# Optimization experiments

Measured on AMD Instinct MI355X. Metric: run time of the kernel, lower is better.

## Reference

```python
import jax, jax.numpy as jnp
import numpy as np

VOCAB, D, TYPES = 100000, 128, 128
T, B = 409600, 8192

def setup_inputs() -> dict:
    key = jax.random.key(0)
    k1, k2, k3, k4 = jax.random.split(key, 4)
    feature_seq = jax.random.randint(k1, (T,), 0, VOCAB, dtype=jnp.int64 if jax.config.read('jax_enable_x64') else jnp.int32)
    offset_seq = jnp.sort(jax.random.randint(k2, (B,), 0, T, dtype=feature_seq.dtype))
    offset_seq = offset_seq.at[0].set(0)  # torch EmbeddingBag requires offsets[0] == 0
    W = jax.random.normal(k3, (VOCAB, D), dtype=jnp.float32) * 0.1
    L = jax.random.normal(k4, (TYPES, 2 * D), dtype=jnp.float32) * 0.05
    return {"feature_seq": feature_seq, "offset_seq": offset_seq, "W": W, "L": L}

def reference(feature_seq, offset_seq, W, L):
    n_tok = feature_seq.shape[0]
    n_bag = offset_seq.shape[0]
    # map each token position to its bag id (offsets are sorted bag starts)
    seg = jnp.searchsorted(offset_seq, jnp.arange(n_tok), side='right') - 1  # [T]
    emb = W[feature_seq]                                                     # [T, D] gather
    counts = jax.ops.segment_sum(jnp.ones((n_tok,), W.dtype), seg, num_segments=n_bag)  # [B]
    ssum = jax.ops.segment_sum(emb, seg, num_segments=n_bag)                 # [B, D]
    mean = ssum / jnp.maximum(counts, 1.0)[:, None]
    smax = jax.ops.segment_max(emb, seg, num_segments=n_bag)                 # [B, D]
    smax = jnp.where(counts[:, None] > 0, smax, 0.0)                         # empty bags -> 0
    men = jnp.concatenate([mean, smax], axis=-1)                             # [B, 2D]
    # dropout is identity in eval mode; linear has no bias
    return men @ L.T                                                         # [B, TYPES]
```

## Files before the change

kernel.cpp:

```cpp
#include <hip/hip_runtime.h>
#include <cfloat>


constexpr int D     = 128;
constexpr int TYPES = 128;
constexpr int BPB   = 4;
constexpr int WPB   = 2;
constexpr int BLOCK = 512;

__global__ __launch_bounds__(BLOCK, 8)
void embbag_men_linear(const int* __restrict__ feat,
                       const int* __restrict__ offs,
                       const float* __restrict__ W,
                       const float* __restrict__ L,
                       float* __restrict__ out,
                       int T, int B)
{
    __shared__ float4 men[BPB][64];
    __shared__ float4 redS[BPB][WPB][32];
    __shared__ float4 redM[BPB][WPB][32];
    __shared__ float  partial[3][BPB][TYPES];

    const int tid  = threadIdx.x;
    const int wv   = tid >> 6;
    const int lane = tid & 63;
    const int bi   = wv >> 1;
    const int wh   = wv & 1;
    const int slot = lane >> 5;
    const int g    = lane & 31;
    const int bag0 = blockIdx.x * BPB;
    const int bag  = bag0 + bi;

    int start = 0, end = 0;
    if (bag < B) {
        start = offs[bag];
        end   = (bag + 1 < B) ? offs[bag + 1] : T;
    }
    const int n  = end - start;
    const int q  = wh * 2 + slot;
    const int qa = start + (n * q) / 4;
    const int qb = start + (n * (q + 1)) / 4;

    float4 s4 = make_float4(0.f, 0.f, 0.f, 0.f);
    float4 m4 = make_float4(-FLT_MAX, -FLT_MAX, -FLT_MAX, -FLT_MAX);
    const float* __restrict__ Wg = W + 4 * g;

    int i = qa;
    for (; i + 8 <= qb; i += 8) {
        int idx[8];
        #pragma unroll
        for (int j = 0; j < 8; ++j) idx[j] = feat[i + j];
        float4 v[8];
        #pragma unroll
        for (int j = 0; j < 8; ++j)
            v[j] = *reinterpret_cast<const float4*>(Wg + (size_t)idx[j] * D);
        #pragma unroll
        for (int j = 0; j < 8; ++j) {
            s4.x += v[j].x; s4.y += v[j].y; s4.z += v[j].z; s4.w += v[j].w;
            m4.x = fmaxf(m4.x, v[j].x); m4.y = fmaxf(m4.y, v[j].y);
            m4.z = fmaxf(m4.z, v[j].z); m4.w = fmaxf(m4.w, v[j].w);
        }
    }
    for (; i < qb; ++i) {
        const int idx = feat[i];
        const float4 v = *reinterpret_cast<const float4*>(Wg + (size_t)idx * D);
        s4.x += v.x; s4.y += v.y; s4.z += v.z; s4.w += v.w;
        m4.x = fmaxf(m4.x, v.x); m4.y = fmaxf(m4.y, v.y);
        m4.z = fmaxf(m4.z, v.z); m4.w = fmaxf(m4.w, v.w);
    }

    s4.x += __shfl_xor(s4.x, 32); s4.y += __shfl_xor(s4.y, 32);
    s4.z += __shfl_xor(s4.z, 32); s4.w += __shfl_xor(s4.w, 32);
    m4.x = fmaxf(m4.x, __shfl_xor(m4.x, 32));
    m4.y = fmaxf(m4.y, __shfl_xor(m4.y, 32));
    m4.z = fmaxf(m4.z, __shfl_xor(m4.z, 32));
    m4.w = fmaxf(m4.w, __shfl_xor(m4.w, 32));

    if (lane < 32) {
        redS[bi][wh][g] = s4;
        redM[bi][wh][g] = m4;
    }
    __syncthreads();

    if (wh == 0 && lane < 32) {
        const float4 a0 = redS[bi][0][g], a1 = redS[bi][1][g];
        const float4 b0 = redM[bi][0][g], b1 = redM[bi][1][g];
        const bool  empty = (n <= 0);
        const float inv   = 1.0f / (float)(empty ? 1 : n);
        men[bi][g] = make_float4((a0.x + a1.x) * inv, (a0.y + a1.y) * inv,
                                 (a0.z + a1.z) * inv, (a0.w + a1.w) * inv);
        men[bi][32 + g] = empty
            ? make_float4(0.f, 0.f, 0.f, 0.f)
            : make_float4(fmaxf(b0.x, b1.x), fmaxf(b0.y, b1.y),
                          fmaxf(b0.z, b1.z), fmaxf(b0.w, b1.w));
    }
    __syncthreads();

    const int o = tid & (TYPES - 1);
    const int h = tid >> 7;

    float acc[BPB];
    #pragma unroll
    for (int b = 0; b < BPB; ++b) acc[b] = 0.f;

    const float* Lrow = L + (size_t)o * (2 * D) + h * 64;
    #pragma unroll
    for (int k4 = 0; k4 < 16; ++k4) {
        const float4 lv = *reinterpret_cast<const float4*>(Lrow + 4 * k4);
        #pragma unroll
        for (int b = 0; b < BPB; ++b) {
            const float4 mv = men[b][h * 16 + k4];
            acc[b] = fmaf(lv.x, mv.x, acc[b]);
            acc[b] = fmaf(lv.y, mv.y, acc[b]);
            acc[b] = fmaf(lv.z, mv.z, acc[b]);
            acc[b] = fmaf(lv.w, mv.w, acc[b]);
        }
    }

    if (h > 0) {
        #pragma unroll
        for (int b = 0; b < BPB; ++b) partial[h - 1][b][o] = acc[b];
    }
    __syncthreads();
    if (h == 0) {
        #pragma unroll
        for (int b = 0; b < BPB; ++b) {
            const int bg = bag0 + b;
            if (bg < B)
                out[(size_t)bg * TYPES + o] =
                    acc[b] + partial[0][b][o] + partial[1][b][o] + partial[2][b][o];
        }
    }
}

extern "C" void kernel_launch(void* const* d_in, const int* in_sizes, int n_in,
                              void* d_out, int out_size, void* d_ws, size_t ws_size,
                              hipStream_t stream)
{
    const int*   feat = (const int*)d_in[0];
    const int*   offs = (const int*)d_in[1];
    const float* W    = (const float*)d_in[2];
    const float* L    = (const float*)d_in[3];
    float*       out  = (float*)d_out;

    const int T = in_sizes[0];
    const int B = in_sizes[1];
    const int grid = (B + BPB - 1) / BPB;
    embbag_men_linear<<<grid, BLOCK, 0, stream>>>(feat, offs, W, L, out, T, B);
}
```

Measured before the change: 67.06 us.

## Split into token-parallel gather with atomics and separate linear kernel

Replaces the bag-per-block fused kernel with a three-step pipeline. A memset clears the workspace, then a token-parallel gather kernel gives each wave 64 tokens, walks bag boundaries, and accumulates sum and max into workspace through atomicAdd and an ordered-integer atomicMax. A second kernel computes the mean and max vectors and applies the linear layer, handling 8 bags per block. The aim is to fix load imbalance from uneven bag sizes, at the cost of atomic traffic, extra workspace round trips and two extra launches. The old fused kernel stays as a fallback when the workspace is too small.

```diff
diff --git a/kernel.cpp b/kernel.cpp
--- a/kernel.cpp
+++ b/kernel.cpp
@@ -4,61 +4,213 @@
 
 constexpr int D     = 128;
 constexpr int TYPES = 128;
-constexpr int BPB   = 4;
-constexpr int WPB   = 2;
-constexpr int BLOCK = 512;
-
-__global__ __launch_bounds__(BLOCK, 8)
-void embbag_men_linear(const int* __restrict__ feat,
-                       const int* __restrict__ offs,
-                       const float* __restrict__ W,
-                       const float* __restrict__ L,
-                       float* __restrict__ out,
-                       int T, int B)
+constexpr int TPW   = 64;
+constexpr int K2BPB = 8;
+
+__device__ __forceinline__ unsigned fkey(float f) {
+    unsigned b = __float_as_uint(f);
+    return (b & 0x80000000u) ? ~b : (b | 0x80000000u);
+}
+__device__ __forceinline__ float funkey(unsigned k) {
+    return __uint_as_float((k & 0x80000000u) ? (k & 0x7FFFFFFFu) : ~k);
+}
+
+__global__ __launch_bounds__(256, 8)
+void k1_gather(const int* __restrict__ feat, const int* __restrict__ offs,
+               const float* __restrict__ W,
+               float* __restrict__ wsum, unsigned* __restrict__ wkey,
+               int T, int B)
 {
-    __shared__ float4 men[BPB][64];
-    __shared__ float4 redS[BPB][WPB][32];
-    __shared__ float4 redM[BPB][WPB][32];
-    __shared__ float  partial[3][BPB][TYPES];
-
-    const int tid  = threadIdx.x;
-    const int wv   = tid >> 6;
-    const int lane = tid & 63;
-    const int bi   = wv >> 1;
-    const int wh   = wv & 1;
+    const int wave = (blockIdx.x << 2) + (threadIdx.x >> 6);
+    const int lane = threadIdx.x & 63;
     const int slot = lane >> 5;
     const int g    = lane & 31;
-    const int bag0 = blockIdx.x * BPB;
-    const int bag  = bag0 + bi;
-
-    int start = 0, end = 0;
-    if (bag < B) {
-        start = offs[bag];
-        end   = (bag + 1 < B) ? offs[bag + 1] : T;
-    }
-    const int n  = end - start;
-    const int q  = wh * 2 + slot;
-    const int qa = start + (n * q) / 4;
-    const int qb = start + (n * (q + 1)) / 4;
-
+    const int i0   = wave * TPW;
+    if (i0 >= T) return;
+    const int iend = min(i0 + TPW, T);
+
+    int lo = 0, hi = B;
+    while (lo < hi) {
+        const int mid = (lo + hi) >> 1;
+        if (offs[mid] <= i0) lo = mid + 1; else hi = mid;
+    }
+    int seg    = lo - 1;
+    int segEnd = (seg + 1 < B) ? offs[seg + 1] : T;
+
+    const float* __restrict__ Wg = W + 4 * g;
     float4 s4 = make_float4(0.f, 0.f, 0.f, 0.f);
     float4 m4 = make_float4(-FLT_MAX, -FLT_MAX, -FLT_MAX, -FLT_MAX);
-    const float* __restrict__ Wg = W + 4 * g;
-
+    bool dirty = false;
+    int i = i0;
+
+    while (true) {
+        const int stop = min(iend, segEnd);
+        int len = stop - i;
+        if (len > 0) {
+            dirty = true;
+            for (; len >= 16; len -= 16, i += 16) {
+                int idx[8];
+                #pragma unroll
+                for (int u = 0; u < 8; ++u) idx[u] = feat[i + 2 * u + slot];
+                float4 v[8];
+                #pragma unroll
+                for (int u = 0; u < 8; ++u)
+                    v[u] = *reinterpret_cast<const float4*>(Wg + (size_t)idx[u] * D);
+                #pragma unroll
+                for (int u = 0; u < 8; ++u) {
+                    s4.x += v[u].x; s4.y += v[u].y;
+                    s4.z += v[u].z; s4.w += v[u].w;
+                    m4.x = fmaxf(m4.x, v[u].x); m4.y = fmaxf(m4.y, v[u].y);
+                    m4.z = fmaxf(m4.z, v[u].z); m4.w = fmaxf(m4.w, v[u].w);
+                }
+            }
+            if (len > 0) {
+                int idx[8];
+                #pragma unroll
+                for (int u = 0; u < 8; ++u) {
+                    const int t = i + 2 * u + slot;
+                    idx[u] = feat[t < stop ? t : stop - 1];
+                }
+                float4 v[8];
+                #pragma unroll
+                for (int u = 0; u < 8; ++u)
+                    v[u] = *reinterpret_cast<const float4*>(Wg + (size_t)idx[u] * D);
+                #pragma unroll
+                for (int u = 0; u < 8; ++u) {
+                    const bool val = (i + 2 * u + slot) < stop;
+                    s4.x += val ? v[u].x : 0.f;
+                    s4.y += val ? v[u].y : 0.f;
+                    s4.z += val ? v[u].z : 0.f;
+                    s4.w += val ? v[u].w : 0.f;
+                    m4.x = fmaxf(m4.x, val ? v[u].x : -FLT_MAX);
+                    m4.y = fmaxf(m4.y, val ? v[u].y : -FLT_MAX);
+                    m4.z = fmaxf(m4.z, val ? v[u].z : -FLT_MAX);
+                    m4.w = fmaxf(m4.w, val ? v[u].w : -FLT_MAX);
+                }
+                i = stop;
+            }
+        }
+
+        const bool done = (i >= iend);
+        if (dirty && (done || i >= segEnd)) {
+            s4.x += __shfl_xor(s4.x, 32); s4.y += __shfl_xor(s4.y, 32);
+            s4.z += __shfl_xor(s4.z, 32); s4.w += __shfl_xor(s4.w, 32);
+            m4.x = fmaxf(m4.x, __shfl_xor(m4.x, 32));
+            m4.y = fmaxf(m4.y, __shfl_xor(m4.y, 32));
+            m4.z = fmaxf(m4.z, __shfl_xor(m4.z, 32));
+            m4.w = fmaxf(m4.w, __shfl_xor(m4.w, 32));
+            if (lane < 32) {
+                float* ps = wsum + (size_t)seg * D + 4 * g;
+                atomicAdd(ps + 0, s4.x); atomicAdd(ps + 1, s4.y);
+                atomicAdd(ps + 2, s4.z); atomicAdd(ps + 3, s4.w);
+                unsigned* pk = wkey + (size_t)seg * D + 4 * g;
+                atomicMax(pk + 0, fkey(m4.x)); atomicMax(pk + 1, fkey(m4.y));
+                atomicMax(pk + 2, fkey(m4.z)); atomicMax(pk + 3, fkey(m4.w));
+            }
+            s4 = make_float4(0.f, 0.f, 0.f, 0.f);
+            m4 = make_float4(-FLT_MAX, -FLT_MAX, -FLT_MAX, -FLT_MAX);
+            dirty = false;
+        }
+        if (done) break;
+        ++seg;
+        segEnd = (seg + 1 < B) ? offs[seg + 1] : T;
+    }
+}
+
+__global__ __launch_bounds__(256, 8)
+void k2_linear(const int* __restrict__ offs,
+               const float* __restrict__ wsum, const unsigned* __restrict__ wkey,
+               const float* __restrict__ L, float* __restrict__ out,
+               int T, int B)
+{
+    __shared__ float men[K2BPB][2 * D];
+    __shared__ float partial[K2BPB][TYPES];
+    const int tid  = threadIdx.x;
+    const int bag0 = blockIdx.x * K2BPB;
+
+    for (int e = tid; e < K2BPB * 2 * D; e += 256) {
+        const int r   = e >> 8;
+        const int j   = e & 255;
+        const int bag = bag0 + r;
+        float v = 0.f;
+        if (bag < B) {
+            const int st  = offs[bag];
+            const int en  = (bag + 1 < B) ? offs[bag + 1] : T;
+            const int cnt = en - st;
+            if (cnt > 0) {
+                if (j < D) v = wsum[(size_t)bag * D + j] / (float)cnt;
+                else       v = funkey(wkey[(size_t)bag * D + (j - D)]);
+            }
+        }
+        men[r][j] = v;
+    }
+    __syncthreads();
+
+    const int o = tid & (TYPES - 1);
+    const int h = tid >> 7;
+    float acc[K2BPB];
+    #pragma unroll
+    for (int b = 0; b < K2BPB; ++b) acc[b] = 0.f;
+
+    const float* Lrow = L + (size_t)o * (2 * D) + h * D;
+    #pragma unroll 4
+    for (int k4 = 0; k4 < D / 4; ++k4) {
+        const float4 lv = *reinterpret_cast<const float4*>(Lrow + 4 * k4);
+        #pragma unroll
+        for (int b = 0; b < K2BPB; ++b) {
+            const float4 mv = *reinterpret_cast<const float4*>(&men[b][h * D + 4 * k4]);
+            acc[b] = fmaf(lv.x, mv.x, acc[b]);
+            acc[b] = fmaf(lv.y, mv.y, acc[b]);
+            acc[b] = fmaf(lv.z, mv.z, acc[b]);
+            acc[b] = fmaf(lv.w, mv.w, acc[b]);
+        }
+    }
+    if (h == 1) {
+        #pragma unroll
+        for (int b = 0; b < K2BPB; ++b) partial[b][o] = acc[b];
+    }
+    __syncthreads();
+    if (h == 0) {
+        #pragma unroll
+        for (int b = 0; b < K2BPB; ++b) {
+            const int bag = bag0 + b;
+            if (bag < B)
+                out[(size_t)bag * TYPES + o] = acc[b] + partial[b][o];
+        }
+    }
+}
+
+constexpr int FBPB = 4;
+__global__ __launch_bounds__(512, 8)
+void embbag_fallback(const int* __restrict__ feat, const int* __restrict__ offs,
+                     const float* __restrict__ W, const float* __restrict__ L,
+                     float* __restrict__ out, int T, int B)
+{
+    __shared__ float4 men[FBPB][64];
+    __shared__ float4 redS[FBPB][2][32];
+    __shared__ float4 redM[FBPB][2][32];
+    __shared__ float  partial[3][FBPB][TYPES];
+    const int tid = threadIdx.x, wv = tid >> 6, lane = tid & 63;
+    const int bi = wv >> 1, wh = wv & 1, slot = lane >> 5, g = lane & 31;
+    const int bag0 = blockIdx.x * FBPB, bag = bag0 + bi;
+    int start = 0, end = 0;
+    if (bag < B) { start = offs[bag]; end = (bag + 1 < B) ? offs[bag + 1] : T; }
+    const int n = end - start, q = wh * 2 + slot;
+    const int qa = start + (n * q) / 4, qb = start + (n * (q + 1)) / 4;
+    float4 s4 = make_float4(0.f, 0.f, 0.f, 0.f);
+    float4 m4 = make_float4(-FLT_MAX, -FLT_MAX, -FLT_MAX, -FLT_MAX);
+    const float* Wg = W + 4 * g;
     int i = qa;
     for (; i + 8 <= qb; i += 8) {
         int idx[8];
         #pragma unroll
         for (int j = 0; j < 8; ++j) idx[j] = feat[i + j];
-        float4 v[8];
-        #pragma unroll
-        for (int j = 0; j < 8; ++j)
-            v[j] = *reinterpret_cast<const float4*>(Wg + (size_t)idx[j] * D);
         #pragma unroll
         for (int j = 0; j < 8; ++j) {
-            s4.x += v[j].x; s4.y += v[j].y; s4.z += v[j].z; s4.w += v[j].w;
-            m4.x = fmaxf(m4.x, v[j].x); m4.y = fmaxf(m4.y, v[j].y);
-            m4.z = fmaxf(m4.z, v[j].z); m4.w = fmaxf(m4.w, v[j].w);
+            const float4 v = *reinterpret_cast<const float4*>(Wg + (size_t)idx[j] * D);
+            s4.x += v.x; s4.y += v.y; s4.z += v.z; s4.w += v.w;
+            m4.x = fmaxf(m4.x, v.x); m4.y = fmaxf(m4.y, v.y);
+            m4.z = fmaxf(m4.z, v.z); m4.w = fmaxf(m4.w, v.w);
         }
     }
     for (; i < qb; ++i) {
@@ -68,47 +220,36 @@
         m4.x = fmaxf(m4.x, v.x); m4.y = fmaxf(m4.y, v.y);
         m4.z = fmaxf(m4.z, v.z); m4.w = fmaxf(m4.w, v.w);
     }
-
     s4.x += __shfl_xor(s4.x, 32); s4.y += __shfl_xor(s4.y, 32);
     s4.z += __shfl_xor(s4.z, 32); s4.w += __shfl_xor(s4.w, 32);
     m4.x = fmaxf(m4.x, __shfl_xor(m4.x, 32));
     m4.y = fmaxf(m4.y, __shfl_xor(m4.y, 32));
     m4.z = fmaxf(m4.z, __shfl_xor(m4.z, 32));
     m4.w = fmaxf(m4.w, __shfl_xor(m4.w, 32));
-
-    if (lane < 32) {
-        redS[bi][wh][g] = s4;
-        redM[bi][wh][g] = m4;
-    }
-    __syncthreads();
-
+    if (lane < 32) { redS[bi][wh][g] = s4; redM[bi][wh][g] = m4; }
+    __syncthreads();
     if (wh == 0 && lane < 32) {
         const float4 a0 = redS[bi][0][g], a1 = redS[bi][1][g];
         const float4 b0 = redM[bi][0][g], b1 = redM[bi][1][g];
-        const bool  empty = (n <= 0);
-        const float inv   = 1.0f / (float)(empty ? 1 : n);
-        men[bi][g] = make_float4((a0.x + a1.x) * inv, (a0.y + a1.y) * inv,
-                                 (a0.z + a1.z) * inv, (a0.w + a1.w) * inv);
-        men[bi][32 + g] = empty
-            ? make_float4(0.f, 0.f, 0.f, 0.f)
-            : make_float4(fmaxf(b0.x, b1.x), fmaxf(b0.y, b1.y),
-                          fmaxf(b0.z, b1.z), fmaxf(b0.w, b1.w));
-    }
-    __syncthreads();
-
-    const int o = tid & (TYPES - 1);
-    const int h = tid >> 7;
-
-    float acc[BPB];
+        const bool empty = (n <= 0);
+        const float inv = 1.0f / (float)(empty ? 1 : n);
+        men[bi][g] = make_float4((a0.x+a1.x)*inv, (a0.y+a1.y)*inv,
+                                 (a0.z+a1.z)*inv, (a0.w+a1.w)*inv);
+        men[bi][32+g] = empty ? make_float4(0.f,0.f,0.f,0.f)
+            : make_float4(fmaxf(b0.x,b1.x), fmaxf(b0.y,b1.y),
+                          fmaxf(b0.z,b1.z), fmaxf(b0.w,b1.w));
+    }
+    __syncthreads();
+    const int o = tid & (TYPES - 1), h = tid >> 7;
+    float acc[FBPB];
     #pragma unroll
-    for (int b = 0; b < BPB; ++b) acc[b] = 0.f;
-
+    for (int b = 0; b < FBPB; ++b) acc[b] = 0.f;
     const float* Lrow = L + (size_t)o * (2 * D) + h * 64;
     #pragma unroll
     for (int k4 = 0; k4 < 16; ++k4) {
         const float4 lv = *reinterpret_cast<const float4*>(Lrow + 4 * k4);
         #pragma unroll
-        for (int b = 0; b < BPB; ++b) {
+        for (int b = 0; b < FBPB; ++b) {
             const float4 mv = men[b][h * 16 + k4];
             acc[b] = fmaf(lv.x, mv.x, acc[b]);
             acc[b] = fmaf(lv.y, mv.y, acc[b]);
@@ -116,18 +257,17 @@
             acc[b] = fmaf(lv.w, mv.w, acc[b]);
         }
     }
-
     if (h > 0) {
         #pragma unroll
-        for (int b = 0; b < BPB; ++b) partial[h - 1][b][o] = acc[b];
+        for (int b = 0; b < FBPB; ++b) partial[h-1][b][o] = acc[b];
     }
     __syncthreads();
     if (h == 0) {
         #pragma unroll
-        for (int b = 0; b < BPB; ++b) {
+        for (int b = 0; b < FBPB; ++b) {
             const int bg = bag0 + b;
             if (bg < B)
-                out[(size_t)bg * TYPES + o] =
+                out[(size_t)bg*TYPES+o] =
                     acc[b] + partial[0][b][o] + partial[1][b][o] + partial[2][b][o];
         }
     }
@@ -142,9 +282,24 @@
     const float* W    = (const float*)d_in[2];
     const float* L    = (const float*)d_in[3];
     float*       out  = (float*)d_out;
-
     const int T = in_sizes[0];
     const int B = in_sizes[1];
-    const int grid = (B + BPB - 1) / BPB;
-    embbag_men_linear<<<grid, BLOCK, 0, stream>>>(feat, offs, W, L, out, T, B);
-}
+
+    const size_t need = (size_t)B * D * (sizeof(float) + sizeof(unsigned));
+    if (ws_size < need) {
+        const int grid = (B + FBPB - 1) / FBPB;
+        embbag_fallback<<<grid, 512, 0, stream>>>(feat, offs, W, L, out, T, B);
+        return;
+    }
+
+    float*    wsum = (float*)d_ws;
+    unsigned* wkey = (unsigned*)((char*)d_ws + (size_t)B * D * sizeof(float));
+    (void)hipMemsetAsync(d_ws, 0, need, stream);
+
+    const int nwave = (T + TPW - 1) / TPW;
+    const int grid1 = (nwave + 3) / 4;
+    k1_gather<<<grid1, 256, 0, stream>>>(feat, offs, W, wsum, wkey, T, B);
+
+    const int grid2 = (B + K2BPB - 1) / K2BPB;
+    k2_linear<<<grid2, 256, 0, stream>>>(offs, wsum, wkey, L, out, T, B);
+}
```

Measured after the change: 103.8 us. 54.7% more time.

## Balance token work across waves per block with shared-memory atomic bag reduction

Applied to the files above, without the earlier changes.

Each block now handles 8 bags and splits their combined token range evenly across all 8 waves, instead of pinning two waves to each bag. This removes the load imbalance caused by varying bag lengths. Partial sums and maxima are merged through LDS atomics, with the max done as an ordered unsigned key. Feature indices are loaded once per 64-token chunk and broadcast with shuffles. The cost is more complex segment-crossing logic plus atomic contention, and halving the grid size reduces the number of blocks available to hide latency.

```diff
diff --git a/kernel.cpp b/kernel.cpp
--- a/kernel.cpp
+++ b/kernel.cpp
@@ -4,101 +4,161 @@
 
 constexpr int D     = 128;
 constexpr int TYPES = 128;
-constexpr int BPB   = 4;
-constexpr int WPB   = 2;
+constexpr int BPB   = 8;
 constexpr int BLOCK = 512;
+constexpr int WPB   = BLOCK / 64;
+
+__device__ __forceinline__ unsigned fkey(float f) {
+    unsigned b = __float_as_uint(f);
+    return (b & 0x80000000u) ? ~b : (b | 0x80000000u);
+}
+__device__ __forceinline__ float funkey(unsigned k) {
+    return __uint_as_float((k & 0x80000000u) ? (k & 0x7FFFFFFFu) : ~k);
+}
 
 __global__ __launch_bounds__(BLOCK, 8)
-void embbag_men_linear(const int* __restrict__ feat,
-                       const int* __restrict__ offs,
-                       const float* __restrict__ W,
-                       const float* __restrict__ L,
-                       float* __restrict__ out,
-                       int T, int B)
+void embbag_fused(const int* __restrict__ feat, const int* __restrict__ offs,
+                  const float* __restrict__ W, const float* __restrict__ L,
+                  float* __restrict__ out, int T, int B)
 {
-    __shared__ float4 men[BPB][64];
-    __shared__ float4 redS[BPB][WPB][32];
-    __shared__ float4 redM[BPB][WPB][32];
-    __shared__ float  partial[3][BPB][TYPES];
+    __shared__ int      soffs[BPB + 1];
+    __shared__ float    ssum[BPB][D];
+    __shared__ unsigned skey[BPB][D];
+    __shared__ float    partial[3][BPB][TYPES];
 
     const int tid  = threadIdx.x;
     const int wv   = tid >> 6;
     const int lane = tid & 63;
-    const int bi   = wv >> 1;
-    const int wh   = wv & 1;
     const int slot = lane >> 5;
     const int g    = lane & 31;
     const int bag0 = blockIdx.x * BPB;
-    const int bag  = bag0 + bi;
-
-    int start = 0, end = 0;
-    if (bag < B) {
-        start = offs[bag];
-        end   = (bag + 1 < B) ? offs[bag + 1] : T;
-    }
-    const int n  = end - start;
-    const int q  = wh * 2 + slot;
-    const int qa = start + (n * q) / 4;
-    const int qb = start + (n * (q + 1)) / 4;
-
-    float4 s4 = make_float4(0.f, 0.f, 0.f, 0.f);
-    float4 m4 = make_float4(-FLT_MAX, -FLT_MAX, -FLT_MAX, -FLT_MAX);
-    const float* __restrict__ Wg = W + 4 * g;
-
-    int i = qa;
-    for (; i + 8 <= qb; i += 8) {
-        int idx[8];
-        #pragma unroll
-        for (int j = 0; j < 8; ++j) idx[j] = feat[i + j];
-        float4 v[8];
-        #pragma unroll
-        for (int j = 0; j < 8; ++j)
-            v[j] = *reinterpret_cast<const float4*>(Wg + (size_t)idx[j] * D);
-        #pragma unroll
-        for (int j = 0; j < 8; ++j) {
-            s4.x += v[j].x; s4.y += v[j].y; s4.z += v[j].z; s4.w += v[j].w;
-            m4.x = fmaxf(m4.x, v[j].x); m4.y = fmaxf(m4.y, v[j].y);
-            m4.z = fmaxf(m4.z, v[j].z); m4.w = fmaxf(m4.w, v[j].w);
+
+    if (tid <= BPB) {
+        const int bg = bag0 + tid;
+        soffs[tid] = (bg < B) ? offs[bg] : T;
+    }
+    for (int e = tid; e < BPB * D; e += BLOCK) {
+        (&ssum[0][0])[e] = 0.f;
+        (&skey[0][0])[e] = 0u;
+    }
+    __syncthreads();
+
+    const int tstart = soffs[0];
+    const int nT     = soffs[BPB] - tstart;
+
+    const int c_lo = tstart + (int)(((long long)nT * wv) / WPB);
+    const int c_hi = tstart + (int)(((long long)nT * (wv + 1)) / WPB);
+
+    if (c_lo < c_hi) {
+        int seg = 0;
+        while (seg < BPB - 1 && soffs[seg + 1] <= c_lo) ++seg;
+        int segEnd = soffs[seg + 1];
+
+        const float* __restrict__ Wg = W + 4 * g;
+
+        for (int c0 = c_lo; c0 < c_hi; c0 += 64) {
+            const int iend   = min(c0 + 64, c_hi);
+            const int idxreg = feat[min(c0 + lane, T - 1)];
+
+            float4 s4 = make_float4(0.f, 0.f, 0.f, 0.f);
+            float4 m4 = make_float4(-FLT_MAX, -FLT_MAX, -FLT_MAX, -FLT_MAX);
+            bool dirty = false;
+            int i = c0;
+
+            while (true) {
+                const int stop = min(iend, segEnd);
+                int len = stop - i;
+                if (len > 0) {
+                    dirty = true;
+                    for (; len >= 16; len -= 16, i += 16) {
+                        int idx[8];
+                        #pragma unroll
+                        for (int u = 0; u < 8; ++u)
+                            idx[u] = __shfl(idxreg, (i - c0) + 2 * u + slot);
+                        float4 v[8];
+                        #pragma unroll
+                        for (int u = 0; u < 8; ++u)
+                            v[u] = *reinterpret_cast<const float4*>(
+                                       Wg + (size_t)idx[u] * D);
+                        #pragma unroll
+                        for (int u = 0; u < 8; ++u) {
+                            s4.x += v[u].x; s4.y += v[u].y;
+                            s4.z += v[u].z; s4.w += v[u].w;
+                            m4.x = fmaxf(m4.x, v[u].x);
+                            m4.y = fmaxf(m4.y, v[u].y);
+                            m4.z = fmaxf(m4.z, v[u].z);
+                            m4.w = fmaxf(m4.w, v[u].w);
+                        }
+                    }
+                    if (len > 0) {
+                        int idx[8]; bool val[8];
+                        #pragma unroll
+                        for (int u = 0; u < 8; ++u) {
+                            const int t = i + 2 * u + slot;
+                            val[u] = (t < stop);
+                            idx[u] = __shfl(idxreg, (val[u] ? t : stop - 1) - c0);
+                        }
+                        float4 v[8];
+                        #pragma unroll
+                        for (int u = 0; u < 8; ++u)
+                            v[u] = *reinterpret_cast<const float4*>(
+                                       Wg + (size_t)idx[u] * D);
+                        #pragma unroll
+                        for (int u = 0; u < 8; ++u) {
+                            s4.x += val[u] ? v[u].x : 0.f;
+                            s4.y += val[u] ? v[u].y : 0.f;
+                            s4.z += val[u] ? v[u].z : 0.f;
+                            s4.w += val[u] ? v[u].w : 0.f;
+                            m4.x = fmaxf(m4.x, val[u] ? v[u].x : -FLT_MAX);
+                            m4.y = fmaxf(m4.y, val[u] ? v[u].y : -FLT_MAX);
+                            m4.z = fmaxf(m4.z, val[u] ? v[u].z : -FLT_MAX);
+                            m4.w = fmaxf(m4.w, val[u] ? v[u].w : -FLT_MAX);
+                        }
+                        i = stop;
+                    }
+                }
+
+                const bool done = (i >= iend);
+                if (dirty && (done || i >= segEnd)) {
+                    s4.x += __shfl_xor(s4.x, 32); s4.y += __shfl_xor(s4.y, 32);
+                    s4.z += __shfl_xor(s4.z, 32); s4.w += __shfl_xor(s4.w, 32);
+                    m4.x = fmaxf(m4.x, __shfl_xor(m4.x, 32));
+                    m4.y = fmaxf(m4.y, __shfl_xor(m4.y, 32));
+                    m4.z = fmaxf(m4.z, __shfl_xor(m4.z, 32));
+                    m4.w = fmaxf(m4.w, __shfl_xor(m4.w, 32));
+                    const float a0 = slot ? s4.z : s4.x;
+                    const float a1 = slot ? s4.w : s4.y;
+                    const float b0 = slot ? m4.z : m4.x;
+                    const float b1 = slot ? m4.w : m4.y;
+                    const int j = 4 * g + 2 * slot;
+                    atomicAdd(&ssum[seg][j],     a0);
+                    atomicAdd(&ssum[seg][j + 1], a1);
+                    atomicMax(&skey[seg][j],     fkey(b0));
+                    atomicMax(&skey[seg][j + 1], fkey(b1));
+                    s4 = make_float4(0.f, 0.f, 0.f, 0.f);
+                    m4 = make_float4(-FLT_MAX, -FLT_MAX, -FLT_MAX, -FLT_MAX);
+                    dirty = false;
+                }
+                if (done) break;
+                seg = min(seg + 1, BPB - 1);
+                segEnd = soffs[seg + 1];
+            }
         }
     }
-    for (; i < qb; ++i) {
-        const int idx = feat[i];
-        const float4 v = *reinterpret_cast<const float4*>(Wg + (size_t)idx * D);
-        s4.x += v.x; s4.y += v.y; s4.z += v.z; s4.w += v.w;
-        m4.x = fmaxf(m4.x, v.x); m4.y = fmaxf(m4.y, v.y);
-        m4.z = fmaxf(m4.z, v.z); m4.w = fmaxf(m4.w, v.w);
-    }
-
-    s4.x += __shfl_xor(s4.x, 32); s4.y += __shfl_xor(s4.y, 32);
-    s4.z += __shfl_xor(s4.z, 32); s4.w += __shfl_xor(s4.w, 32);
-    m4.x = fmaxf(m4.x, __shfl_xor(m4.x, 32));
-    m4.y = fmaxf(m4.y, __shfl_xor(m4.y, 32));
-    m4.z = fmaxf(m4.z, __shfl_xor(m4.z, 32));
-    m4.w = fmaxf(m4.w, __shfl_xor(m4.w, 32));
-
-    if (lane < 32) {
-        redS[bi][wh][g] = s4;
-        redM[bi][wh][g] = m4;
-    }
-    __syncthreads();
-
-    if (wh == 0 && lane < 32) {
-        const float4 a0 = redS[bi][0][g], a1 = redS[bi][1][g];
-        const float4 b0 = redM[bi][0][g], b1 = redM[bi][1][g];
-        const bool  empty = (n <= 0);
-        const float inv   = 1.0f / (float)(empty ? 1 : n);
-        men[bi][g] = make_float4((a0.x + a1.x) * inv, (a0.y + a1.y) * inv,
-                                 (a0.z + a1.z) * inv, (a0.w + a1.w) * inv);
-        men[bi][32 + g] = empty
-            ? make_float4(0.f, 0.f, 0.f, 0.f)
-            : make_float4(fmaxf(b0.x, b1.x), fmaxf(b0.y, b1.y),
-                          fmaxf(b0.z, b1.z), fmaxf(b0.w, b1.w));
+    __syncthreads();
+
+    for (int e = tid; e < BPB * D; e += BLOCK) {
+        const int b   = e >> 7;
+        const int cnt = soffs[b + 1] - soffs[b];
+        const float inv = 1.0f / (float)max(cnt, 1);
+        (&ssum[0][0])[e] *= inv;
+        const float mx = (cnt > 0) ? funkey((&skey[0][0])[e]) : 0.f;
+        reinterpret_cast<float*>(&skey[0][0])[e] = mx;
     }
     __syncthreads();
 
     const int o = tid & (TYPES - 1);
     const int h = tid >> 7;
-
     float acc[BPB];
     #pragma unroll
     for (int b = 0; b < BPB; ++b) acc[b] = 0.f;
@@ -109,7 +169,9 @@
         const float4 lv = *reinterpret_cast<const float4*>(Lrow + 4 * k4);
         #pragma unroll
         for (int b = 0; b < BPB; ++b) {
-            const float4 mv = men[b][h * 16 + k4];
+            const float4 mv = (h < 2)
+                ? reinterpret_cast<const float4*>(&ssum[b][0])[h * 16 + k4]
+                : reinterpret_cast<const float4*>(&skey[b][0])[(h - 2) * 16 + k4];
             acc[b] = fmaf(lv.x, mv.x, acc[b]);
             acc[b] = fmaf(lv.y, mv.y, acc[b]);
             acc[b] = fmaf(lv.z, mv.z, acc[b]);
@@ -125,9 +187,9 @@
     if (h == 0) {
         #pragma unroll
         for (int b = 0; b < BPB; ++b) {
-            const int bg = bag0 + b;
-            if (bg < B)
-                out[(size_t)bg * TYPES + o] =
+            const int bag = bag0 + b;
+            if (bag < B)
+                out[(size_t)bag * TYPES + o] =
                     acc[b] + partial[0][b][o] + partial[1][b][o] + partial[2][b][o];
         }
     }
@@ -142,9 +204,9 @@
     const float* W    = (const float*)d_in[2];
     const float* L    = (const float*)d_in[3];
     float*       out  = (float*)d_out;
-
     const int T = in_sizes[0];
     const int B = in_sizes[1];
+
     const int grid = (B + BPB - 1) / BPB;
-    embbag_men_linear<<<grid, BLOCK, 0, stream>>>(feat, offs, W, L, out, T, B);
-}
+    embbag_fused<<<grid, BLOCK, 0, stream>>>(feat, offs, W, L, out, T, B);
+}
```

Result: no change. 66.02 us (-1.6%).
